# Kernel tuning notes

Hardware: AMD Instinct MI355X
Metric: run time of the kernel (lower is better)

## Reference

```python
import jax, jax.numpy as jnp
import numpy as np

N = 20000      # nodes
E = 320000     # edges (avg degree 16)
G = 256        # graphs
F_NODE = 64
F_EDGE = 16
HID = 256
H, C = 4, 64   # heads, per-head channels
EPS = 1e-5


def setup_inputs() -> dict:
    key = jax.random.key(0)
    ks = jax.random.split(key, 24)
    def rn(k, shape, scale=0.05):
        return jax.random.normal(k, shape, dtype=jnp.float32) * scale
    src = jax.random.randint(ks[0], (E,), 0, N)
    dst = (src + 1 + jax.random.randint(ks[1], (E,), 0, N - 1)) % N  # no pre-existing self loops
    edge_index = jnp.stack([src, dst]).astype(jnp.int32)
    batch = ((jnp.arange(N) * G) // N).astype(jnp.int32)  # contiguous graph ids, all G graphs non-empty
    return {
        'x': rn(ks[2], (N, F_NODE), 1.0),
        'edge_index': edge_index,
        'batch': batch,
        'edge_attr': rn(ks[3], (E, F_EDGE), 1.0),
        'enc_W': rn(ks[4], (F_NODE, HID)),
        'enc_b': jnp.zeros((HID,), jnp.float32),
        'conv_Wl': rn(ks[5], (3, HID, HID)),
        'conv_bl': rn(ks[6], (3, HID)),
        'conv_Wr': rn(ks[7], (3, HID, HID)),
        'conv_br': rn(ks[8], (3, HID)),
        'conv_We': rn(ks[9], (3, F_EDGE, HID)),
        'conv_att': rn(ks[10], (3, H, C)),
        'conv_bias': rn(ks[11], (3, HID)),
        'bn_gamma': jnp.ones((3, HID), jnp.float32),
        'bn_beta': jnp.zeros((3, HID), jnp.float32),
        'bn_mean': rn(ks[12], (3, HID)),
        'bn_var': jax.random.uniform(ks[13], (3, HID), dtype=jnp.float32) + 0.5,
        'cls_W1': rn(ks[14], (2 * HID, HID)),
        'cls_b1': jnp.zeros((HID,), jnp.float32),
        'cls_g1': jnp.ones((HID,), jnp.float32),
        'cls_bt1': jnp.zeros((HID,), jnp.float32),
        'cls_m1': rn(ks[15], (HID,)),
        'cls_v1': jax.random.uniform(ks[16], (HID,), dtype=jnp.float32) + 0.5,
        'cls_W2': rn(ks[17], (HID, HID // 2)),
        'cls_b2': jnp.zeros((HID // 2,), jnp.float32),
        'cls_g2': jnp.ones((HID // 2,), jnp.float32),
        'cls_bt2': jnp.zeros((HID // 2,), jnp.float32),
        'cls_m2': rn(ks[18], (HID // 2,)),
        'cls_v2': jax.random.uniform(ks[19], (HID // 2,), dtype=jnp.float32) + 0.5,
        'cls_W3': rn(ks[20], (HID // 2, 1)),
        'cls_b3': jnp.zeros((1,), jnp.float32),
    }


def _bn(v, g, b, m, var):
    return (v - m) * jax.lax.rsqrt(var + EPS) * g + b


def _gatv2(h, src, dst, eattr, Wl, bl, Wr, br, We, att, bias, n):
    # GATv2Conv (share_weights=False, concat=True) with edge features.
    xl = (h @ Wl + bl).reshape(n, H, C)          # messages come from lin_l(source)
    xr = (h @ Wr + br).reshape(n, H, C)
    ef = (eattr @ We).reshape(-1, H, C)
    z = jax.nn.leaky_relu(xl[src] + xr[dst] + ef, 0.2)   # [E', H, C]
    alpha = jnp.einsum('ehc,hc->eh', z, att)             # [E', H]
    amax = jax.ops.segment_max(alpha, dst, num_segments=n)
    amax = jnp.where(jnp.isfinite(amax), amax, 0.0)
    ex = jnp.exp(alpha - amax[dst])
    den = jax.ops.segment_sum(ex, dst, num_segments=n)
    a = ex / den[dst]                                    # self loops guarantee den > 0
    out = jax.ops.segment_sum(a[:, :, None] * xl[src], dst, num_segments=n)
    return out.reshape(n, H * C) + bias


def reference(x, edge_index, batch, edge_attr, enc_W, enc_b, conv_Wl, conv_bl, conv_Wr, conv_br, conv_We, conv_att, conv_bias, bn_gamma, bn_beta, bn_mean, bn_var, cls_W1, cls_b1, cls_g1, cls_bt1, cls_m1, cls_v1, cls_W2, cls_b2, cls_g2, cls_bt2, cls_m2, cls_v2, cls_W3, cls_b3):
    n = x.shape[0]
    src, dst = edge_index[0], edge_index[1]
    # add self loops with fill_value='mean' (mean of incoming edge_attr per node)
    deg = jax.ops.segment_sum(jnp.ones(src.shape, x.dtype), dst, num_segments=n)
    loop_attr = jax.ops.segment_sum(edge_attr, dst, num_segments=n) / jnp.maximum(deg, 1.0)[:, None]
    loop = jnp.arange(n, dtype=src.dtype)
    src2 = jnp.concatenate([src, loop])
    dst2 = jnp.concatenate([dst, loop])
    ea2 = jnp.concatenate([edge_attr, loop_attr], axis=0)

    h = jax.nn.relu(x @ enc_W + enc_b)
    for i in range(3):  # fixed layer count
        h_in = h
        hc = _gatv2(h, src2, dst2, ea2, conv_Wl[i], conv_bl[i], conv_Wr[i], conv_br[i], conv_We[i], conv_att[i], conv_bias[i], n)
        h = jax.nn.relu(_bn(hc, bn_gamma[i], bn_beta[i], bn_mean[i], bn_var[i])) + h_in

    cnt = jax.ops.segment_sum(jnp.ones((n,), h.dtype), batch, num_segments=G)
    x_mean = jax.ops.segment_sum(h, batch, num_segments=G) / jnp.maximum(cnt, 1.0)[:, None]
    x_max = jax.ops.segment_max(h, batch, num_segments=G)
    xp = jnp.concatenate([x_mean, x_max], axis=1)

    z = jax.nn.relu(_bn(xp @ cls_W1 + cls_b1, cls_g1, cls_bt1, cls_m1, cls_v1))
    z = jax.nn.relu(_bn(z @ cls_W2 + cls_b2, cls_g2, cls_bt2, cls_m2, cls_v2))
    return (z @ cls_W3 + cls_b3)[:, 0]
```

## Files before the change

kernel.cpp:

```cpp
#include <hip/hip_runtime.h>
#include <hip/hip_bf16.h>

#define N_NODES 20000
#define N_EDGES 320000
#define N_E2    (N_EDGES + N_NODES)
#define N_GRAPHS 256
#define HID 256
#define EPS 1e-5f
#define NSCAN 20
#define CPB 8

typedef unsigned short u16;
typedef __attribute__((ext_vector_type(8))) short short8;
typedef __attribute__((ext_vector_type(4))) float f32x4;

__device__ __forceinline__ float b2f(u16 u) {
    union { unsigned int i; float f; } v; v.i = ((unsigned int)u) << 16; return v.f;
}
__device__ __forceinline__ u16 f2b(float f) {
    __hip_bfloat16 h = __float2bfloat16(f);
    return *reinterpret_cast<u16*>(&h);
}

__global__ void k_init(int* cnt, int* cursor) {
    int i = blockIdx.x * 256 + threadIdx.x;
    if (i < N_NODES) { cnt[i] = 1; cursor[i] = 0; }
}

__global__ void k_count(const int* __restrict__ dst, int* __restrict__ cnt) {
    int e = blockIdx.x * 256 + threadIdx.x;
    if (e < N_EDGES) atomicAdd(&cnt[dst[e]], 1);
}

__global__ void k_scan1(const int* __restrict__ cnt, int* __restrict__ rowp, int* __restrict__ part) {
    __shared__ int ls[256];
    int b = blockIdx.x, tid = threadIdx.x;
    int base = b * 1024 + tid * 4;
    int c[4]; int s = 0;
#pragma unroll
    for (int u = 0; u < 4; u++) { int i = base + u; c[u] = (i < N_NODES) ? cnt[i] : 0; s += c[u]; }
    ls[tid] = s; __syncthreads();
    for (int off = 1; off < 256; off <<= 1) {
        int v = (tid >= off) ? ls[tid - off] : 0;
        __syncthreads();
        ls[tid] += v;
        __syncthreads();
    }
    int excl = ls[tid] - s;
#pragma unroll
    for (int u = 0; u < 4; u++) { int i = base + u; if (i < N_NODES) rowp[i] = excl; excl += c[u]; }
    if (tid == 255) part[b] = ls[255];
}

__global__ void k_scan2(int* part, int* rowp) {
    int s = 0;
    for (int b = 0; b < NSCAN; b++) { int v = part[b]; part[b] = s; s += v; }
    rowp[N_NODES] = s;
}

__global__ void k_scan3(int* __restrict__ rowp, const int* __restrict__ part) {
    int b = blockIdx.x, tid = threadIdx.x;
    int add = part[b];
    int base = b * 1024 + tid * 4;
#pragma unroll
    for (int u = 0; u < 4; u++) { int i = base + u; if (i < N_NODES) rowp[i] += add; }
}

__global__ void k_fill(const int* __restrict__ src, const int* __restrict__ dst,
                       const int* __restrict__ rowp, int* __restrict__ cursor,
                       int* __restrict__ csr_src, int* __restrict__ csr_dst,
                       int* __restrict__ csr_aid) {
    int t = blockIdx.x * 256 + threadIdx.x;
    if (t < N_EDGES) {
        int d = dst[t];
        int pos = atomicAdd(&cursor[d], 1);
        int w = rowp[d] + pos;
        csr_src[w] = src[t];
        csr_dst[w] = d;
        csr_aid[w] = t;
    } else if (t < N_E2) {
        int n = t - N_EDGES;
        int pos = atomicAdd(&cursor[n], 1);
        int w = rowp[n] + pos;
        csr_src[w] = n;
        csr_dst[w] = n;
        csr_aid[w] = N_EDGES + n;
    }
}

__global__ void k_pad(int* csr_src, int* csr_dst) {
    int i = threadIdx.x;
    csr_src[N_E2 + i] = 0;
    csr_dst[N_E2 + i] = 0;
}

__global__ void k_loopattr(const int* __restrict__ rowp, const int* __restrict__ csr_aid,
                           const float* __restrict__ edge_attr, float* __restrict__ lattr) {
    int t = blockIdx.x * 256 + threadIdx.x;
    if (t >= N_NODES * 16) return;
    int n = t >> 4, j = t & 15;
    int st = rowp[n], en = rowp[n + 1];
    float s = 0.f;
    for (int i = st; i < en; i++) {
        int aid = csr_aid[i];
        if (aid < N_EDGES) s += edge_attr[(size_t)aid * 16 + j];
    }
    float deg = (float)(en - st - 1);
    lattr[(size_t)n * 16 + j] = s / fmaxf(deg, 1.0f);
}

__global__ void k_eacsr(const int* __restrict__ csr_aid,
                        const float* __restrict__ edge_attr,
                        const float* __restrict__ lattr,
                        u16* __restrict__ ea_bf) {
    int t = blockIdx.x * 256 + threadIdx.x;
    if (t >= N_E2 * 2) return;
    int e = t >> 1, hf = t & 1;
    int aid = csr_aid[e];
    const float* ap = (aid < N_EDGES) ? edge_attr + (size_t)aid * 16
                                      : lattr + (size_t)(aid - N_EDGES) * 16;
    float4 a = ((const float4*)ap)[hf * 2];
    float4 b = ((const float4*)ap)[hf * 2 + 1];
    u16 v[8] = {f2b(a.x), f2b(a.y), f2b(a.z), f2b(a.w),
                f2b(b.x), f2b(b.y), f2b(b.z), f2b(b.w)};
    *(uint4*)(ea_bf + (size_t)t * 8) = *(uint4*)v;
}

__global__ void k_wef(const float* __restrict__ We, u16* __restrict__ Wef) {
    int t = blockIdx.x * 256 + threadIdx.x;
    if (t >= 3 * 16 * 64) return;
    int layer = t >> 10, r = t & 1023;
    int nt = r >> 6, l = r & 63;
    int kc = l >> 4, ch = nt * 16 + (l & 15);
    u16 v[8];
#pragma unroll
    for (int q = 0; q < 8; q++) {
        float x = 0.f;
        if (kc < 2) x = We[(size_t)layer * 4096 + (size_t)(kc * 8 + q) * 256 + ch];
        v[q] = f2b(x);
    }
    *(uint4*)(Wef + (size_t)t * 8) = *(uint4*)v;
}

__global__ void k_xbf(const float* __restrict__ x, u16* __restrict__ xb) {
    int t = blockIdx.x * 256 + threadIdx.x;
    if (t >= N_NODES * 16) return;
    float4 v = ((const float4*)x)[t];
    u16 o[4] = {f2b(v.x), f2b(v.y), f2b(v.z), f2b(v.w)};
    *(ushort4*)(xb + (size_t)t * 4) = *(ushort4*)o;
}

__global__ void k_twg(const float* __restrict__ W, u16* __restrict__ Wt, int K, int N) {
    __shared__ float tile[32][33];
    int layer = blockIdx.z;
    const float* Wp = W + (size_t)layer * K * N;
    u16* Wtp = Wt + (size_t)layer * K * N;
    int bk = blockIdx.x * 32, bn = blockIdx.y * 32;
    int tx = threadIdx.x & 31, ty = threadIdx.x >> 5;
#pragma unroll
    for (int q = 0; q < 4; q++) {
        int k = bk + ty + q * 8;
        tile[ty + q * 8][tx] = Wp[(size_t)k * N + bn + tx];
    }
    __syncthreads();
#pragma unroll
    for (int q = 0; q < 4; q++) {
        int n = bn + ty + q * 8;
        Wtp[(size_t)n * K + bk + tx] = f2b(tile[tx][ty + q * 8]);
    }
}

template <int EPI>
__global__ __launch_bounds__(256) void k_gemm_bf(
    const u16* __restrict__ A, int lda,
    const u16* __restrict__ Bt, int ldb, int K,
    const float* __restrict__ bias,
    u16* __restrict__ Cbf, int ldc, int coff,
    float* __restrict__ Cf, int M)
{
    __shared__ __align__(16) u16 As[128 * 40];
    __shared__ __align__(16) u16 Bs[64 * 40];
    int tid = threadIdx.x;
    int lane = tid & 63, w = tid >> 6;
    int m0 = blockIdx.x * 128, n0 = blockIdx.y * 64;

    f32x4 acc[2][4];
#pragma unroll
    for (int i = 0; i < 2; i++)
#pragma unroll
        for (int j = 0; j < 4; j++) acc[i][j] = (f32x4){0.f, 0.f, 0.f, 0.f};

    int srow = tid >> 2, skc = (tid & 3) * 8;
    int lr = lane & 15, lk = (lane >> 4) * 8;

    int ktiles = K >> 5;
    for (int kt = 0; kt < ktiles; kt++) {
        if (kt) __syncthreads();
#pragma unroll
        for (int q = 0; q < 2; q++) {
            int arow = q * 64 + srow;
            uint4 av = make_uint4(0, 0, 0, 0);
            if (m0 + arow < M)
                av = *(const uint4*)(A + (size_t)(m0 + arow) * lda + kt * 32 + skc);
            *(uint4*)&As[arow * 40 + skc] = av;
        }
        {
            uint4 bv = *(const uint4*)(Bt + (size_t)(n0 + srow) * ldb + kt * 32 + skc);
            *(uint4*)&Bs[srow * 40 + skc] = bv;
        }
        __syncthreads();

        short8 af0 = *(const short8*)&As[(w * 32 + lr) * 40 + lk];
        short8 af1 = *(const short8*)&As[(w * 32 + 16 + lr) * 40 + lk];
        short8 bf[4];
#pragma unroll
        for (int nt = 0; nt < 4; nt++)
            bf[nt] = *(const short8*)&Bs[(nt * 16 + lr) * 40 + lk];
#pragma unroll
        for (int nt = 0; nt < 4; nt++) {
            acc[0][nt] = __builtin_amdgcn_mfma_f32_16x16x32_bf16(af0, bf[nt], acc[0][nt], 0, 0, 0);
            acc[1][nt] = __builtin_amdgcn_mfma_f32_16x16x32_bf16(af1, bf[nt], acc[1][nt], 0, 0, 0);
        }
    }

    int rq = (lane >> 4) * 4;
#pragma unroll
    for (int nt = 0; nt < 4; nt++) {
        int col = n0 + nt * 16 + lr;
        float bv = bias[col];
#pragma unroll
        for (int mt = 0; mt < 2; mt++) {
#pragma unroll
            for (int j = 0; j < 4; j++) {
                int row = m0 + w * 32 + mt * 16 + rq + j;
                if (row < M) {
                    float v = acc[mt][nt][j] + bv;
                    if (EPI == 1) {
                        v = fmaxf(v, 0.f);
                        Cf[(size_t)row * ldc + col] = v;
                        Cbf[(size_t)row * ldc + col] = f2b(v);
                    } else {
                        Cbf[(size_t)row * ldc + coff + col] = f2b(v);
                    }
                }
            }
        }
    }
}

__global__ __launch_bounds__(256) void k_alpha3(
    const u16* __restrict__ xlr,
    const u16* __restrict__ ea_bf,
    const int* __restrict__ csr_src, const int* __restrict__ csr_dst,
    const u16* __restrict__ Wef,
    const float* __restrict__ att,
    float* __restrict__ alpha)
{
    __shared__ __align__(16) u16 wef_s[16 * 64 * 8];
    __shared__ float att_s[256];
    int tid = threadIdx.x, lane = tid & 63, w = tid >> 6;
    {
        const uint4* s = (const uint4*)Wef;
        uint4* d = (uint4*)wef_s;
#pragma unroll
        for (int q = 0; q < 4; q++) d[q * 256 + tid] = s[q * 256 + tid];
        att_s[tid] = att[tid];
    }
    int eg = lane >> 4, t16 = lane & 15;
    __syncthreads();

    for (int it = 0; it < CPB; it++) {
        int chunk = blockIdx.x * CPB + it;
        if (chunk * 64 >= N_E2) break;
        int e_base = chunk * 64 + w * 16;
        int e_raw = e_base + t16;
        int e = (e_raw < N_E2) ? e_raw : N_E2 - 1;

        short8 eafrag = {0, 0, 0, 0, 0, 0, 0, 0};
        if (eg < 2) eafrag = *(const short8*)(ea_bf + (size_t)e * 16 + eg * 8);
        int s = csr_src[e], d = csr_dst[e];
        const u16* xlp = xlr + (size_t)s * 512;
        const u16* xrp = xlr + (size_t)d * 512 + 256;

        float pj = 0.f;
#pragma unroll
        for (int nt = 0; nt < 16; nt++) {
            short8 wfrag = *(const short8*)&wef_s[(nt * 64 + lane) * 8];
            f32x4 D = __builtin_amdgcn_mfma_f32_16x16x32_bf16(
                wfrag, eafrag, (f32x4){0.f, 0.f, 0.f, 0.f}, 0, 0, 0);
            int ch0 = nt * 16 + eg * 4;
            ushort4 xl4 = *(const ushort4*)(xlp + ch0);
            ushort4 xr4 = *(const ushort4*)(xrp + ch0);
            float4 at4 = *(const float4*)&att_s[ch0];
#pragma unroll
            for (int j = 0; j < 4; j++) {
                float z = D[j] + b2f(((const u16*)&xl4)[j]) + b2f(((const u16*)&xr4)[j]);
                z = fmaxf(z, 0.f) + 0.2f * fminf(z, 0.f);
                pj = fmaf(z, ((const float*)&at4)[j], pj);
            }
            if ((nt & 3) == 3) {
                float p = pj;
                p += __shfl_xor(p, 16, 64);
                p += __shfl_xor(p, 32, 64);
                if (eg == 0 && e_raw < N_E2) alpha[(size_t)e_raw * 4 + (nt >> 2)] = p;
                pj = 0.f;
            }
        }
    }
}

__global__ __launch_bounds__(256) void k_aggr(
    const u16* __restrict__ xlr, const float* __restrict__ alpha,
    const int* __restrict__ rowp, const int* __restrict__ csr_src,
    const float* __restrict__ cbias,
    const float* __restrict__ bng, const float* __restrict__ bnb,
    const float* __restrict__ bnm, const float* __restrict__ bnv,
    float* __restrict__ h, u16* __restrict__ h_bf)
{
    __shared__ float lex[4][64][4];
    __shared__ int   lsrc[4][64];
    int lane = threadIdx.x & 63;
    int wv = threadIdx.x >> 6;
    int n = blockIdx.x * 4 + wv;
    if (n >= N_NODES) return;
    int st = rowp[n], en = rowp[n + 1];
    int hsel = lane >> 4;
    int c0 = lane * 4;

    float m4[4]  = {-3.0e38f, -3.0e38f, -3.0e38f, -3.0e38f};
    float den4[4] = {0.f, 0.f, 0.f, 0.f};
    float acc[4]  = {0.f, 0.f, 0.f, 0.f};

    for (int cs = st; cs < en; cs += 64) {
        int cnt = min(64, en - cs);
        float a4[4];
        int s_i = 0;
        if (lane < cnt) {
            float4 v = *(const float4*)(alpha + (size_t)(cs + lane) * 4);
            a4[0] = v.x; a4[1] = v.y; a4[2] = v.z; a4[3] = v.w;
            s_i = csr_src[cs + lane];
        } else {
            a4[0] = a4[1] = a4[2] = a4[3] = -3.0e38f;
        }
        float cm[4] = {a4[0], a4[1], a4[2], a4[3]};
#pragma unroll
        for (int o = 32; o >= 1; o >>= 1)
#pragma unroll
            for (int u = 0; u < 4; u++) cm[u] = fmaxf(cm[u], __shfl_xor(cm[u], o, 64));
        float sc[4];
#pragma unroll
        for (int u = 0; u < 4; u++) {
            float nm = fmaxf(m4[u], cm[u]);
            sc[u] = __expf(m4[u] - nm);
            den4[u] *= sc[u];
            m4[u] = nm;
        }
        float scl = sc[hsel];
#pragma unroll
        for (int u = 0; u < 4; u++) acc[u] *= scl;
        float ex[4];
#pragma unroll
        for (int u = 0; u < 4; u++) ex[u] = (lane < cnt) ? __expf(a4[u] - m4[u]) : 0.f;
        float sx[4] = {ex[0], ex[1], ex[2], ex[3]};
#pragma unroll
        for (int o = 32; o >= 1; o >>= 1)
#pragma unroll
            for (int u = 0; u < 4; u++) sx[u] += __shfl_xor(sx[u], o, 64);
#pragma unroll
        for (int u = 0; u < 4; u++) den4[u] += sx[u];
        *(float4*)&lex[wv][lane][0] = make_float4(ex[0], ex[1], ex[2], ex[3]);
        lsrc[wv][lane] = s_i;
        int j = 0;
        for (; j + 8 <= cnt; j += 8) {
            float a[8]; int sj[8];
#pragma unroll
            for (int q = 0; q < 8; q++) { a[q] = lex[wv][j + q][hsel]; sj[q] = lsrc[wv][j + q]; }
            ushort4 xg[8];
#pragma unroll
            for (int q = 0; q < 8; q++) xg[q] = *(const ushort4*)(xlr + (size_t)sj[q] * 512 + c0);
#pragma unroll
            for (int q = 0; q < 8; q++) {
                acc[0] += a[q] * b2f(((const u16*)&xg[q])[0]);
                acc[1] += a[q] * b2f(((const u16*)&xg[q])[1]);
                acc[2] += a[q] * b2f(((const u16*)&xg[q])[2]);
                acc[3] += a[q] * b2f(((const u16*)&xg[q])[3]);
            }
        }
        for (; j < cnt; j++) {
            float a = lex[wv][j][hsel];
            int sj = lsrc[wv][j];
            ushort4 xg = *(const ushort4*)(xlr + (size_t)sj * 512 + c0);
            acc[0] += a * b2f(((const u16*)&xg)[0]);
            acc[1] += a * b2f(((const u16*)&xg)[1]);
            acc[2] += a * b2f(((const u16*)&xg)[2]);
            acc[3] += a * b2f(((const u16*)&xg)[3]);
        }
    }

    float dd = den4[hsel];
    float4 hin = *(const float4*)(h + (size_t)n * 256 + c0);
    float4 cb  = *(const float4*)(cbias + c0);
    float4 gg  = *(const float4*)(bng + c0);
    float4 bb  = *(const float4*)(bnb + c0);
    float4 mm  = *(const float4*)(bnm + c0);
    float4 vv  = *(const float4*)(bnv + c0);
    float hi[4] = {hin.x, hin.y, hin.z, hin.w};
    float cbv[4] = {cb.x, cb.y, cb.z, cb.w};
    float gv[4] = {gg.x, gg.y, gg.z, gg.w};
    float bv[4] = {bb.x, bb.y, bb.z, bb.w};
    float mv[4] = {mm.x, mm.y, mm.z, mm.w};
    float vvv[4] = {vv.x, vv.y, vv.z, vv.w};
    float4 o;
    ushort4 ob;
#pragma unroll
    for (int u = 0; u < 4; u++) {
        float val = acc[u] / dd + cbv[u];
        val = (val - mv[u]) * rsqrtf(vvv[u] + EPS) * gv[u] + bv[u];
        val = fmaxf(val, 0.f) + hi[u];
        ((float*)&o)[u] = val;
        ((u16*)&ob)[u] = f2b(val);
    }
    *(float4*)(h + (size_t)n * 256 + c0) = o;
    *(ushort4*)(h_bf + (size_t)n * 256 + c0) = ob;
}

__global__ __launch_bounds__(256) void k_poolp(
    const float* __restrict__ h, float* __restrict__ psum, float* __restrict__ pmax)
{
    int g = blockIdx.x, p = blockIdx.y, c = threadIdx.x;
    int gst = (g * N_NODES + N_GRAPHS - 1) / N_GRAPHS;
    int gen = ((g + 1) * N_NODES + N_GRAPHS - 1) / N_GRAPHS;
    int len = gen - gst;
    int cst = gst + (len * p) / 8;
    int cen = gst + (len * (p + 1)) / 8;
    float s = 0.f, mx = -3.0e38f;
    for (int i = cst; i < cen; i++) {
        float v = h[(size_t)i * 256 + c];
        s += v;
        mx = fmaxf(mx, v);
    }
    psum[(size_t)(g * 8 + p) * 256 + c] = s;
    pmax[(size_t)(g * 8 + p) * 256 + c] = mx;
}

__global__ __launch_bounds__(256) void k_head(
    const float* __restrict__ psum, const float* __restrict__ pmax,
    const float* __restrict__ W1, const float* __restrict__ b1,
    const float* __restrict__ g1, const float* __restrict__ bt1,
    const float* __restrict__ m1, const float* __restrict__ v1,
    const float* __restrict__ W2, const float* __restrict__ b2,
    const float* __restrict__ g2, const float* __restrict__ bt2,
    const float* __restrict__ m2, const float* __restrict__ v2,
    const float* __restrict__ W3, const float* __restrict__ b3,
    float* __restrict__ out)
{
    __shared__ float xp_s[512];
    __shared__ float z1_s[256];
    __shared__ float z2p[2][128];
    __shared__ float z2_s[128];
    int g = blockIdx.x, c = threadIdx.x;
    int gst = (g * N_NODES + N_GRAPHS - 1) / N_GRAPHS;
    int gen = ((g + 1) * N_NODES + N_GRAPHS - 1) / N_GRAPHS;

    float s = 0.f, mx = -3.0e38f;
#pragma unroll
    for (int p = 0; p < 8; p++) {
        s += psum[(size_t)(g * 8 + p) * 256 + c];
        mx = fmaxf(mx, pmax[(size_t)(g * 8 + p) * 256 + c]);
    }
    xp_s[c] = s / (float)(gen - gst);
    xp_s[256 + c] = mx;
    __syncthreads();

    float a0 = 0.f, a1 = 0.f, a2 = 0.f, a3 = 0.f;
#pragma unroll 4
    for (int k = 0; k < 512; k += 4) {
        a0 = fmaf(xp_s[k + 0], W1[(k + 0) * 256 + c], a0);
        a1 = fmaf(xp_s[k + 1], W1[(k + 1) * 256 + c], a1);
        a2 = fmaf(xp_s[k + 2], W1[(k + 2) * 256 + c], a2);
        a3 = fmaf(xp_s[k + 3], W1[(k + 3) * 256 + c], a3);
    }
    float a = (a0 + a1) + (a2 + a3) + b1[c];
    a = (a - m1[c]) * rsqrtf(v1[c] + EPS) * g1[c] + bt1[c];
    z1_s[c] = fmaxf(a, 0.f);
    __syncthreads();

    {
        int c2 = c & 127, half = c >> 7;
        float b_acc = 0.f;
#pragma unroll 4
        for (int k = 0; k < 128; k++) {
            int kk = half * 128 + k;
            b_acc = fmaf(z1_s[kk], W2[kk * 128 + c2], b_acc);
        }
        z2p[half][c2] = b_acc;
    }
    __syncthreads();
    if (c < 128) {
        float a2v = z2p[0][c] + z2p[1][c] + b2[c];
        a2v = (a2v - m2[c]) * rsqrtf(v2[c] + EPS) * g2[c] + bt2[c];
        z2_s[c] = fmaxf(a2v, 0.f);
    }
    __syncthreads();

    if (c < 64) {
        float a3v = z2_s[c] * W3[c] + z2_s[c + 64] * W3[c + 64];
#pragma unroll
        for (int o = 32; o >= 1; o >>= 1) a3v += __shfl_xor(a3v, o, 64);
        if (c == 0) out[g] = a3v + b3[0];
    }
}

extern "C" void kernel_launch(void* const* d_in, const int* in_sizes, int n_in,
                              void* d_out, int out_size, void* d_ws, size_t ws_size,
                              hipStream_t stream) {
    const float* x         = (const float*)d_in[0];
    const int*   ei        = (const int*)d_in[1];
    const int*   src       = ei;
    const int*   dst       = ei + N_EDGES;
    const float* edge_attr = (const float*)d_in[3];
    const float* enc_W     = (const float*)d_in[4];
    const float* enc_b     = (const float*)d_in[5];
    const float* conv_Wl   = (const float*)d_in[6];
    const float* conv_bl   = (const float*)d_in[7];
    const float* conv_Wr   = (const float*)d_in[8];
    const float* conv_br   = (const float*)d_in[9];
    const float* conv_We   = (const float*)d_in[10];
    const float* conv_att  = (const float*)d_in[11];
    const float* conv_bias = (const float*)d_in[12];
    const float* bn_g      = (const float*)d_in[13];
    const float* bn_b      = (const float*)d_in[14];
    const float* bn_m      = (const float*)d_in[15];
    const float* bn_v      = (const float*)d_in[16];
    const float* cls_W1    = (const float*)d_in[17];
    const float* cls_b1    = (const float*)d_in[18];
    const float* cls_g1    = (const float*)d_in[19];
    const float* cls_bt1   = (const float*)d_in[20];
    const float* cls_m1    = (const float*)d_in[21];
    const float* cls_v1    = (const float*)d_in[22];
    const float* cls_W2    = (const float*)d_in[23];
    const float* cls_b2    = (const float*)d_in[24];
    const float* cls_g2    = (const float*)d_in[25];
    const float* cls_bt2   = (const float*)d_in[26];
    const float* cls_m2    = (const float*)d_in[27];
    const float* cls_v2    = (const float*)d_in[28];
    const float* cls_W3    = (const float*)d_in[29];
    const float* cls_b3    = (const float*)d_in[30];
    float* out = (float*)d_out;

    char* ws = (char*)d_ws;
    size_t off = 0;
    auto alloc = [&](size_t bytes) -> void* {
        void* p = ws + off;
        off += (bytes + 255) & ~(size_t)255;
        return p;
    };
    float* h       = (float*)alloc((size_t)N_NODES * 256 * 4);
    u16*   h_bf    = (u16*)alloc((size_t)N_NODES * 256 * 2);
    u16*   xlr_bf  = (u16*)alloc((size_t)N_NODES * 512 * 2);
    float* lattr   = (float*)alloc((size_t)N_NODES * 16 * 4);
    u16*   ea_bf   = (u16*)alloc((size_t)N_E2 * 16 * 2);
    float* alphas  = (float*)alloc((size_t)N_E2 * 4 * 4);
    u16*   x_bf    = (u16*)alloc((size_t)N_NODES * 64 * 2);
    u16*   enc_Wt  = (u16*)alloc((size_t)64 * 256 * 2);
    u16*   Wtl     = (u16*)alloc((size_t)3 * 65536 * 2);
    u16*   Wtr     = (u16*)alloc((size_t)3 * 65536 * 2);
    u16*   Wef     = (u16*)alloc((size_t)3 * 16 * 64 * 8 * 2);
    float* psum    = (float*)alloc((size_t)N_GRAPHS * 8 * 256 * 4);
    float* pmax    = (float*)alloc((size_t)N_GRAPHS * 8 * 256 * 4);
    int*   cnt     = (int*)alloc((size_t)N_NODES * 4);
    int*   rowp    = (int*)alloc((size_t)(N_NODES + 1) * 4);
    int*   cursor  = (int*)alloc((size_t)N_NODES * 4);
    int*   csr_src = (int*)alloc((size_t)(N_E2 + 512) * 4);
    int*   csr_dst = (int*)alloc((size_t)(N_E2 + 512) * 4);
    int*   csr_aid = (int*)alloc((size_t)N_E2 * 4);
    int*   part    = (int*)alloc(64 * 4);

    k_init<<<(N_NODES + 255) / 256, 256, 0, stream>>>(cnt, cursor);
    k_count<<<(N_EDGES + 255) / 256, 256, 0, stream>>>(dst, cnt);
    k_scan1<<<NSCAN, 256, 0, stream>>>(cnt, rowp, part);
    k_scan2<<<1, 1, 0, stream>>>(part, rowp);
    k_scan3<<<NSCAN, 256, 0, stream>>>(rowp, part);
    k_fill<<<(N_E2 + 255) / 256, 256, 0, stream>>>(src, dst, rowp, cursor, csr_src, csr_dst, csr_aid);
    k_pad<<<1, 512, 0, stream>>>(csr_src, csr_dst);
    k_loopattr<<<(N_NODES * 16 + 255) / 256, 256, 0, stream>>>(rowp, csr_aid, edge_attr, lattr);
    k_eacsr<<<(N_E2 * 2 + 255) / 256, 256, 0, stream>>>(csr_aid, edge_attr, lattr, ea_bf);

    k_xbf<<<(N_NODES * 16 + 255) / 256, 256, 0, stream>>>(x, x_bf);
    k_twg<<<dim3(2, 8, 1), 256, 0, stream>>>(enc_W, enc_Wt, 64, 256);
    k_twg<<<dim3(8, 8, 3), 256, 0, stream>>>(conv_Wl, Wtl, 256, 256);
    k_twg<<<dim3(8, 8, 3), 256, 0, stream>>>(conv_Wr, Wtr, 256, 256);
    k_wef<<<12, 256, 0, stream>>>(conv_We, Wef);

    dim3 ggrid((N_NODES + 127) / 128, 4);
    k_gemm_bf<1><<<ggrid, 256, 0, stream>>>(x_bf, 64, enc_Wt, 64, 64,
                                            enc_b, h_bf, 256, 0, h, N_NODES);

    int nchunks = (N_E2 + 63) / 64;
    int ablocks = (nchunks + CPB - 1) / CPB;
    for (int i = 0; i < 3; i++) {
        k_gemm_bf<0><<<ggrid, 256, 0, stream>>>(h_bf, 256, Wtl + (size_t)i * 65536, 256, 256,
                                                conv_bl + i * HID, xlr_bf, 512, 0, nullptr, N_NODES);
        k_gemm_bf<0><<<ggrid, 256, 0, stream>>>(h_bf, 256, Wtr + (size_t)i * 65536, 256, 256,
                                                conv_br + i * HID, xlr_bf, 512, 256, nullptr, N_NODES);
        k_alpha3<<<ablocks, 256, 0, stream>>>(
            xlr_bf, ea_bf, csr_src, csr_dst,
            Wef + (size_t)i * 8192, conv_att + (size_t)i * 256, alphas);
        k_aggr<<<N_NODES / 4, 256, 0, stream>>>(
            xlr_bf, alphas, rowp, csr_src,
            conv_bias + (size_t)i * HID,
            bn_g + (size_t)i * HID, bn_b + (size_t)i * HID,
            bn_m + (size_t)i * HID, bn_v + (size_t)i * HID, h, h_bf);
    }

    k_poolp<<<dim3(N_GRAPHS, 8), 256, 0, stream>>>(h, psum, pmax);
    k_head<<<N_GRAPHS, 256, 0, stream>>>(
        psum, pmax, cls_W1, cls_b1, cls_g1, cls_bt1, cls_m1, cls_v1,
        cls_W2, cls_b2, cls_g2, cls_bt2, cls_m2, cls_v2,
        cls_W3, cls_b3, out);
}
```

Before: 496.2 us.

## Merge left/right projection GEMMs, prefetch gathers in alpha kernel, halve chunks per block

Concatenates the Wl and Wr transposed weights and biases so each layer runs a single GEMM with a doubled N grid instead of two launches reading h_bf twice. The alpha kernel now issues all 16 per-edge xl/xr gather loads up front into registers before the MFMA loop, so memory latency overlaps the compute. CPB drops from 8 to 4, which doubles the alpha grid for more parallelism. The register arrays raise VGPR pressure and may lower occupancy.

```diff
diff --git a/kernel.cpp b/kernel.cpp
--- a/kernel.cpp
+++ b/kernel.cpp
@@ -8,7 +8,7 @@
 #define HID 256
 #define EPS 1e-5f
 #define NSCAN 20
-#define CPB 8
+#define CPB 4
 
 typedef unsigned short u16;
 typedef __attribute__((ext_vector_type(8))) short short8;
@@ -150,11 +150,12 @@
     *(ushort4*)(xb + (size_t)t * 4) = *(ushort4*)o;
 }
 
-__global__ void k_twg(const float* __restrict__ W, u16* __restrict__ Wt, int K, int N) {
+__global__ void k_twg(const float* __restrict__ W, u16* __restrict__ Wt, int K, int N,
+                      unsigned int lstride) {
     __shared__ float tile[32][33];
     int layer = blockIdx.z;
     const float* Wp = W + (size_t)layer * K * N;
-    u16* Wtp = Wt + (size_t)layer * K * N;
+    u16* Wtp = Wt + (size_t)layer * lstride;
     int bk = blockIdx.x * 32, bn = blockIdx.y * 32;
     int tx = threadIdx.x & 31, ty = threadIdx.x >> 5;
 #pragma unroll
@@ -168,6 +169,14 @@
         int n = bn + ty + q * 8;
         Wtp[(size_t)n * K + bk + tx] = f2b(tile[tx][ty + q * 8]);
     }
+}
+
+__global__ void k_blr(const float* __restrict__ bl, const float* __restrict__ br,
+                      float* __restrict__ blr) {
+    int t = blockIdx.x * 256 + threadIdx.x;
+    if (t >= 3 * 512) return;
+    int l = t >> 9, c = t & 511;
+    blr[t] = (c < 256) ? bl[l * 256 + c] : br[l * 256 + (c - 256)];
 }
 
 template <int EPI>
@@ -279,8 +288,15 @@
         short8 eafrag = {0, 0, 0, 0, 0, 0, 0, 0};
         if (eg < 2) eafrag = *(const short8*)(ea_bf + (size_t)e * 16 + eg * 8);
         int s = csr_src[e], d = csr_dst[e];
-        const u16* xlp = xlr + (size_t)s * 512;
-        const u16* xrp = xlr + (size_t)d * 512 + 256;
+        const u16* xlp = xlr + (size_t)s * 512 + eg * 4;
+        const u16* xrp = xlr + (size_t)d * 512 + 256 + eg * 4;
+
+        uint2 xlv[16], xrv[16];
+#pragma unroll
+        for (int nt = 0; nt < 16; nt++) {
+            xlv[nt] = *(const uint2*)(xlp + nt * 16);
+            xrv[nt] = *(const uint2*)(xrp + nt * 16);
+        }
 
         float pj = 0.f;
 #pragma unroll
@@ -289,12 +305,12 @@
             f32x4 D = __builtin_amdgcn_mfma_f32_16x16x32_bf16(
                 wfrag, eafrag, (f32x4){0.f, 0.f, 0.f, 0.f}, 0, 0, 0);
             int ch0 = nt * 16 + eg * 4;
-            ushort4 xl4 = *(const ushort4*)(xlp + ch0);
-            ushort4 xr4 = *(const ushort4*)(xrp + ch0);
             float4 at4 = *(const float4*)&att_s[ch0];
+            const u16* xl4 = (const u16*)&xlv[nt];
+            const u16* xr4 = (const u16*)&xrv[nt];
 #pragma unroll
             for (int j = 0; j < 4; j++) {
-                float z = D[j] + b2f(((const u16*)&xl4)[j]) + b2f(((const u16*)&xr4)[j]);
+                float z = D[j] + b2f(xl4[j]) + b2f(xr4[j]);
                 z = fmaxf(z, 0.f) + 0.2f * fminf(z, 0.f);
                 pj = fmaf(z, ((const float*)&at4)[j], pj);
             }
@@ -563,8 +579,8 @@
     float* alphas  = (float*)alloc((size_t)N_E2 * 4 * 4);
     u16*   x_bf    = (u16*)alloc((size_t)N_NODES * 64 * 2);
     u16*   enc_Wt  = (u16*)alloc((size_t)64 * 256 * 2);
-    u16*   Wtl     = (u16*)alloc((size_t)3 * 65536 * 2);
-    u16*   Wtr     = (u16*)alloc((size_t)3 * 65536 * 2);
+    u16*   Wtlr    = (u16*)alloc((size_t)3 * 512 * 256 * 2);
+    float* blr     = (float*)alloc((size_t)3 * 512 * 4);
     u16*   Wef     = (u16*)alloc((size_t)3 * 16 * 64 * 8 * 2);
     float* psum    = (float*)alloc((size_t)N_GRAPHS * 8 * 256 * 4);
     float* pmax    = (float*)alloc((size_t)N_GRAPHS * 8 * 256 * 4);
@@ -587,22 +603,22 @@
     k_eacsr<<<(N_E2 * 2 + 255) / 256, 256, 0, stream>>>(csr_aid, edge_attr, lattr, ea_bf);
 
     k_xbf<<<(N_NODES * 16 + 255) / 256, 256, 0, stream>>>(x, x_bf);
-    k_twg<<<dim3(2, 8, 1), 256, 0, stream>>>(enc_W, enc_Wt, 64, 256);
-    k_twg<<<dim3(8, 8, 3), 256, 0, stream>>>(conv_Wl, Wtl, 256, 256);
-    k_twg<<<dim3(8, 8, 3), 256, 0, stream>>>(conv_Wr, Wtr, 256, 256);
+    k_twg<<<dim3(2, 8, 1), 256, 0, stream>>>(enc_W, enc_Wt, 64, 256, 64 * 256);
+    k_twg<<<dim3(8, 8, 3), 256, 0, stream>>>(conv_Wl, Wtlr, 256, 256, 512 * 256);
+    k_twg<<<dim3(8, 8, 3), 256, 0, stream>>>(conv_Wr, Wtlr + 256 * 256, 256, 256, 512 * 256);
+    k_blr<<<6, 256, 0, stream>>>(conv_bl, conv_br, blr);
     k_wef<<<12, 256, 0, stream>>>(conv_We, Wef);
 
     dim3 ggrid((N_NODES + 127) / 128, 4);
+    dim3 ggrid2((N_NODES + 127) / 128, 8);
     k_gemm_bf<1><<<ggrid, 256, 0, stream>>>(x_bf, 64, enc_Wt, 64, 64,
                                             enc_b, h_bf, 256, 0, h, N_NODES);
 
     int nchunks = (N_E2 + 63) / 64;
     int ablocks = (nchunks + CPB - 1) / CPB;
     for (int i = 0; i < 3; i++) {
-        k_gemm_bf<0><<<ggrid, 256, 0, stream>>>(h_bf, 256, Wtl + (size_t)i * 65536, 256, 256,
-                                                conv_bl + i * HID, xlr_bf, 512, 0, nullptr, N_NODES);
-        k_gemm_bf<0><<<ggrid, 256, 0, stream>>>(h_bf, 256, Wtr + (size_t)i * 65536, 256, 256,
-                                                conv_br + i * HID, xlr_bf, 512, 256, nullptr, N_NODES);
+        k_gemm_bf<0><<<ggrid2, 256, 0, stream>>>(h_bf, 256, Wtlr + (size_t)i * 131072, 256, 256,
+                                                 blr + (size_t)i * 512, xlr_bf, 512, 0, nullptr, N_NODES);
         k_alpha3<<<ablocks, 256, 0, stream>>>(
             xlr_bf, ea_bf, csr_src, csr_dst,
             Wef + (size_t)i * 8192, conv_att + (size_t)i * 256, alphas);
```

Measured after the change: 481.7 us. 2.9% less time.
